# Kernel tuning notes

Measured on AMD Instinct MI355X. Metric: run time of the kernel, lower is better.

## Reference

```python
import jax, jax.numpy as jnp
import numpy as np
import math

N, IN_DIM, Z, H, OUT, K = 16384, 64, 128, 1, 3, 16


def setup_inputs() -> dict:
    key = jax.random.key(0)
    ks = jax.random.split(key, 16)

    def lin(k, din, dout):
        kw, kb = jax.random.split(k)
        W = jax.random.normal(kw, (din, dout), jnp.float32) / math.sqrt(din)
        b = jax.random.normal(kb, (dout,), jnp.float32) * 0.01
        return W, b

    x = jax.random.normal(ks[0], (N, IN_DIM), jnp.float32)
    t = jnp.zeros((1,), jnp.float32)
    # layer dims: (in, heads*out) per TransformerConv
    dims = [(IN_DIM, Z * H), (Z * H, (Z // H) * H), (Z * H, (OUT // H) * H)]
    params = {}
    i = 1
    for li, (din, dout) in enumerate(dims, 1):
        for nm in ("q", "k", "v", "s"):
            W, b = lin(ks[i], din, dout)
            i += 1
            params[f"W{nm}{li}"] = W
            params[f"b{nm}{li}"] = b
    return {"t": t, "x": x, **params}


def knn_edge_index(coo, k):
    # kNN graph on 3-D coords (loop=False): edges neighbor(src) -> center(dst)
    n = coo.shape[0]
    sq = jnp.sum(coo * coo, axis=-1)
    d = sq[:, None] + sq[None, :] - 2.0 * (coo @ coo.T)  # [N, N] sq. distances
    d = d.at[jnp.arange(n), jnp.arange(n)].set(jnp.inf)  # exclude self-loops
    _, idx = jax.lax.top_k(-d, k)  # [N, K] nearest neighbor indices
    src = idx.reshape(-1)
    dst = jnp.repeat(jnp.arange(n), k)
    return src, dst


def tconv(x, src, dst, Wq, bq, Wk, bk, Wv, bv, Ws, bs, heads):
    # PyG TransformerConv (concat=True, root_weight=True, no edge_attr)
    n = x.shape[0]
    dout = Wq.shape[1]
    c = dout // heads
    q = (x @ Wq + bq).reshape(n, heads, c)
    kk = (x @ Wk + bk).reshape(n, heads, c)
    v = (x @ Wv + bv).reshape(n, heads, c)
    alpha = jnp.sum(q[dst] * kk[src], axis=-1) / math.sqrt(c)  # [E, H]
    amax = jax.ops.segment_max(alpha, dst, num_segments=n)
    ex = jnp.exp(alpha - amax[dst])
    denom = jax.ops.segment_sum(ex, dst, num_segments=n)
    w = ex / denom[dst]  # softmax over incoming edges per node
    msg = w[:, :, None] * v[src]  # [E, H, C]
    out = jax.ops.segment_sum(msg, dst, num_segments=n).reshape(n, dout)
    return out + x @ Ws + bs  # root/skip connection


def reference(t, x,
              Wq1, bq1, Wk1, bk1, Wv1, bv1, Ws1, bs1,
              Wq2, bq2, Wk2, bk2, Wv2, bv2, Ws2, bs2,
              Wq3, bq3, Wk3, bk3, Wv3, bv3, Ws3, bs3):
    src, dst = knn_edge_index(x[:, :3], K)  # built under no_grad in original
    h = jnp.tanh(tconv(x, src, dst, Wq1, bq1, Wk1, bk1, Wv1, bv1, Ws1, bs1, H))
    h = jnp.tanh(tconv(h, src, dst, Wq2, bq2, Wk2, bk2, Wv2, bv2, Ws2, bs2, H) + h)
    drift_coo = tconv(h, src, dst, Wq3, bq3, Wk3, bk3, Wv3, bv3, Ws3, bs3, H)
    return drift_coo
```

## Files before the change

kernel.cpp:

```cpp
#include <hip/hip_runtime.h>
#include <math.h>

#define NN 16384
#define CAP 128
#define WM 64
#define KTOP 17
#define NSLAB 128
#define SH 0.0625f
#define SHI 16.0f

typedef unsigned long long u64;

__device__ __forceinline__ int mbcnt64(u64 mask) {
  return __builtin_amdgcn_mbcnt_hi(
      (unsigned)(mask >> 32),
      __builtin_amdgcn_mbcnt_lo((unsigned)mask, 0));
}

__device__ __forceinline__ unsigned fmap(float d) {
  unsigned ub = __float_as_uint(d);
  return ub ^ ((unsigned)((int)ub >> 31) | 0x80000000u);
}

__device__ __forceinline__ float unfmap(unsigned ub) {
  unsigned fb = (ub & 0x80000000u) ? (ub ^ 0x80000000u) : ~ub;
  return __uint_as_float(fb);
}

__device__ __forceinline__ unsigned short f2bf(float f) {
  unsigned u = __float_as_uint(f);
  return (unsigned short)((u + 0x7FFFu + ((u >> 16) & 1u)) >> 16);
}
__device__ __forceinline__ float bf2f(unsigned short h) {
  return __uint_as_float(((unsigned)h) << 16);
}

__device__ __forceinline__ u64 u64min(u64 a, u64 b) { return a < b ? a : b; }
__device__ __forceinline__ u64 u64max(u64 a, u64 b) { return a > b ? a : b; }

__device__ __forceinline__ int slabof(float v) {
  int c = (int)floorf((v + 4.0f) * SHI);
  return c < 0 ? 0 : (c > NSLAB - 1 ? NSLAB - 1 : c);
}

__device__ __forceinline__ void sort64(u64& r0, int lane) {
#pragma unroll
  for (int k = 2; k <= 64; k <<= 1) {
#pragma unroll
    for (int jj = k >> 1; jj >= 1; jj >>= 1) {
      const bool up = (lane & jj) == 0;
      const bool asc = (lane & k) == 0;
      u64 o = __shfl_xor(r0, jj);
      r0 = (up == asc) ? u64min(r0, o) : u64max(r0, o);
    }
  }
}

__device__ __forceinline__ void radix_shrink(u64* buf, int& cnt, float& cq,
                                             int lane) {
  const u64 k0 = (lane < cnt) ? buf[lane] : ~0ull;
  const u64 k1 = (lane + 64 < cnt) ? buf[lane + 64] : ~0ull;
  const unsigned d0 = (unsigned)(k0 >> 32);
  const unsigned d1 = (unsigned)(k1 >> 32);
  unsigned p = 0u;
#pragma unroll
  for (int b = 31; b >= 0; --b) {
    const unsigned c = p | (1u << b);
    const u64 b0 = __ballot(d0 < c);
    const u64 b1 = __ballot(d1 < c);
    const int n = __popcll(b0) + __popcll(b1);
    if (n < KTOP) p = c;
  }
  const bool v0 = d0 <= p;
  const bool v1 = d1 <= p;
  const u64 m0 = __ballot(v0);
  const u64 m1 = __ballot(v1);
  const int base = __popcll(m0);
  if (v0) buf[mbcnt64(m0)] = k0;
  if (v1) buf[base + mbcnt64(m1)] = k1;
  cnt = base + __popcll(m1);
  cq = -unfmap(p);
}

__global__ __launch_bounds__(256) void pack_slabs(const float* __restrict__ x,
                                                  float4* __restrict__ tmp4,
                                                  int* __restrict__ sid,
                                                  unsigned* __restrict__ hist) {
  const int i = blockIdx.x * 256 + threadIdx.x;
  const float a = x[i * 64 + 0];
  const float b = x[i * 64 + 1];
  const float c = x[i * 64 + 2];
  tmp4[i] = make_float4(a, b, c, -0.5f * (a * a + b * b + c * c));
  const int s = slabof(c);
  sid[i] = s;
  atomicAdd(&hist[s], 1u);
}

__global__ __launch_bounds__(128) void prefix_slabs(
    const unsigned* __restrict__ hist, unsigned* __restrict__ slabstart,
    unsigned* __restrict__ slabfill) {
  __shared__ unsigned ls[NSLAB];
  const int t = threadIdx.x;
  const unsigned h = hist[t];
  ls[t] = h;
  __syncthreads();
  for (int off = 1; off < NSLAB; off <<= 1) {
    const unsigned v = (t >= off) ? ls[t - off] : 0u;
    __syncthreads();
    ls[t] += v;
    __syncthreads();
  }
  const unsigned ex = ls[t] - h;
  slabstart[t] = ex;
  slabfill[t] = ex;
  if (t == NSLAB - 1) slabstart[NSLAB] = ls[t];
}

__global__ __launch_bounds__(256) void scatter_slabs(
    const float4* __restrict__ tmp4, const int* __restrict__ sid,
    unsigned* __restrict__ slabfill, float4* __restrict__ sorted4,
    int* __restrict__ sidx) {
  const int i = blockIdx.x * 256 + threadIdx.x;
  const unsigned pos = atomicAdd(&slabfill[sid[i]], 1u);
  sorted4[pos] = tmp4[i];
  sidx[pos] = i;
}

__global__ __launch_bounds__(256) void knn_z(
    const float4* __restrict__ sorted4, const int* __restrict__ sidx,
    const unsigned* __restrict__ slabstart, int* __restrict__ src) {
  __shared__ u64 bufs_[4][CAP];
  const int lane = threadIdx.x & 63;
  const int wid = threadIdx.x >> 6;
  u64* buf = bufs_[wid];
  const int qpos = blockIdx.x * 4 + wid;
  const float4 me = sorted4[qpos];
  const int qorig = sidx[qpos];
  const float qx = me.x, qy = me.y, qz = me.z;
  const float q2 = -2.0f * me.w;
  float cq = -INFINITY;
  int cnt = 0;

  auto scan_run = [&](int s, int e) {
    if (s >= e) return;
    int o = s;
    int j = o + lane;
    float4 p = sorted4[j < e ? j : s];
    while (o < e) {
      const int on = o + 64;
      float4 pn;
      if (on < e) {
        const int jn = on + lane;
        pn = sorted4[jn < e ? jn : s];
      }
      const float L = fmaf(qx, p.x, fmaf(qy, p.y, fmaf(qz, p.z, p.w)));
      const bool pass = (j < e) && (L >= cq);
      const u64 mk = __ballot(pass);
      if (mk) {
        if (pass)
          buf[cnt + mbcnt64(mk)] = ((u64)fmap(-L) << 32) | (unsigned)sidx[j];
        cnt += __popcll(mk);
        if (cnt >= WM) radix_shrink(buf, cnt, cq, lane);
      }
      o = on;
      j = on + lane;
      p = pn;
    }
  };

  const int sq = slabof(qz);
  int su = sq, sd = sq - 1;
  bool up_done = false, dn_done = false;
  while (true) {
    bool can_up = !up_done && su <= NSLAB - 1;
    bool can_dn = !dn_done && sd >= 0;
    float bu = can_up ? fmaxf((-4.0f + su * SH) - qz, 0.0f) : 0.0f;
    float bd = can_dn ? fmaxf(qz - (-4.0f + (sd + 1) * SH), 0.0f) : 0.0f;
    if (cq != -INFINITY) {
      const float d17m =
          fmaxf(fmaf(-2.0f, cq, q2), 0.0f) * 1.00002f + 1e-4f;
      if (can_up && bu * bu > d17m) { can_up = false; up_done = true; }
      if (can_dn && bd * bd > d17m) { can_dn = false; dn_done = true; }
    }
    if (!can_up && !can_dn) {
      if (up_done && dn_done) break;
      if (su > NSLAB - 1 && sd < 0) break;
      if ((up_done || su > NSLAB - 1) && (dn_done || sd < 0)) break;
      break;
    }
    if (can_up && (!can_dn || bu <= bd)) {
      scan_run((int)slabstart[su], (int)slabstart[su + 1]);
      ++su;
    } else {
      scan_run((int)slabstart[sd], (int)slabstart[sd + 1]);
      --sd;
    }
  }

  u64 r0 = (lane < cnt) ? buf[lane] : ~0ull;
  sort64(r0, lane);
  const int idx = (int)(r0 & 0xFFFFFFFFull);
  const u64 selfm = __ballot((lane < KTOP) && (idx == qorig));
  const int sp = selfm ? (__ffsll((long long)selfm) - 1) : 99;
  const int outrank = lane - (lane > sp ? 1 : 0);
  if (lane < KTOP && lane != sp && outrank < 16)
    src[qorig * 16 + outrank] = idx;
}

template <int KD>
__global__ __launch_bounds__(256) void gemm_qkvs(
    const float* __restrict__ X, const float* __restrict__ W0,
    const float* __restrict__ W1, const float* __restrict__ W2,
    const float* __restrict__ W3, const float* __restrict__ B0,
    const float* __restrict__ B1, const float* __restrict__ B2,
    const float* __restrict__ B3, float* __restrict__ qs,
    unsigned short* __restrict__ kvh) {
  __shared__ float As[64][68];
  __shared__ float Bs[64][64];
  const int brow = blockIdx.x * 64;
  const int by = blockIdx.y;
  const int wi = by >> 1;
  const float* W = wi == 0 ? W0 : wi == 1 ? W1 : wi == 2 ? W2 : W3;
  const float* bias = wi == 0 ? B0 : wi == 1 ? B1 : wi == 2 ? B2 : B3;
  const int cbase = (by & 1) * 64;
  const int tx = threadIdx.x & 15;
  const int ty = threadIdx.x >> 4;

  float acc[4][4] = {};
  for (int k0 = 0; k0 < KD; k0 += 64) {
    __syncthreads();
#pragma unroll
    for (int i = 0; i < 4; ++i) {
      const int flat = threadIdx.x * 4 + i * 1024;
      const int r = flat >> 6, kk = flat & 63;
      const float4 v = *(const float4*)&X[(brow + r) * KD + k0 + kk];
      As[kk + 0][r] = v.x;
      As[kk + 1][r] = v.y;
      As[kk + 2][r] = v.z;
      As[kk + 3][r] = v.w;
    }
#pragma unroll
    for (int i = 0; i < 4; ++i) {
      const int flat = threadIdx.x * 4 + i * 1024;
      const int kk = flat >> 6, c = flat & 63;
      *(float4*)&Bs[kk][c] = *(const float4*)&W[(k0 + kk) * 128 + cbase + c];
    }
    __syncthreads();
#pragma unroll 8
    for (int k = 0; k < 64; ++k) {
      const float4 a = *(const float4*)&As[k][ty * 4];
      const float4 b = *(const float4*)&Bs[k][tx * 4];
      const float av[4] = {a.x, a.y, a.z, a.w};
      const float bv[4] = {b.x, b.y, b.z, b.w};
#pragma unroll
      for (int i = 0; i < 4; ++i)
#pragma unroll
        for (int jj = 0; jj < 4; ++jj)
          acc[i][jj] = fmaf(av[i], bv[jj], acc[i][jj]);
    }
  }
  const float4 bi = *(const float4*)&bias[cbase + tx * 4];
  const int col = cbase + tx * 4;
#pragma unroll
  for (int i = 0; i < 4; ++i) {
    const int row = brow + ty * 4 + i;
    float4 o;
    o.x = acc[i][0] + bi.x;
    o.y = acc[i][1] + bi.y;
    o.z = acc[i][2] + bi.z;
    o.w = acc[i][3] + bi.w;
    if (wi == 0) {
      *(float4*)&qs[row * 256 + col] = o;
    } else if (wi == 3) {
      *(float4*)&qs[row * 256 + 128 + col] = o;
    } else {
      ushort4 h;
      h.x = f2bf(o.x);
      h.y = f2bf(o.y);
      h.z = f2bf(o.z);
      h.w = f2bf(o.w);
      *(ushort4*)&kvh[row * 256 + (wi == 1 ? col : 128 + col)] = h;
    }
  }
}

__global__ __launch_bounds__(256) void attn_c128(
    const float* __restrict__ qs, const unsigned short* __restrict__ kvh,
    const int* __restrict__ src, const float* __restrict__ res,
    float* __restrict__ hout, int do_res) {
  const int g = threadIdx.x >> 5;
  const int node = blockIdx.x * 8 + g;
  const int c = threadIdx.x & 31;
  const float4 q4 = ((const float4*)(qs + node * 256))[c];

  int nb[16];
#pragma unroll
  for (int r = 0; r < 16; ++r) nb[r] = src[node * 16 + r];

  float p[16];
#pragma unroll
  for (int r = 0; r < 16; ++r) {
    const ushort4 k4 = ((const ushort4*)(kvh + nb[r] * 256))[c];
    p[r] = q4.x * bf2f(k4.x) + q4.y * bf2f(k4.y) + q4.z * bf2f(k4.z) +
           q4.w * bf2f(k4.w);
  }
#pragma unroll
  for (int o = 16; o; o >>= 1) {
#pragma unroll
    for (int r = 0; r < 16; ++r) p[r] += __shfl_xor(p[r], o);
  }

  float m = p[0];
#pragma unroll
  for (int r = 1; r < 16; ++r) m = fmaxf(m, p[r]);
  float w[16];
  float den = 0.0f;
#pragma unroll
  for (int r = 0; r < 16; ++r) {
    w[r] = __expf((p[r] - m) * 0.088388347648318447f);
    den += w[r];
  }
  const float inv = 1.0f / den;
  float o0 = 0.0f, o1 = 0.0f, o2 = 0.0f, o3 = 0.0f;
#pragma unroll
  for (int r = 0; r < 16; ++r) {
    const ushort4 v4 = ((const ushort4*)(kvh + nb[r] * 256 + 128))[c];
    const float ww = w[r] * inv;
    o0 = fmaf(ww, bf2f(v4.x), o0);
    o1 = fmaf(ww, bf2f(v4.y), o1);
    o2 = fmaf(ww, bf2f(v4.z), o2);
    o3 = fmaf(ww, bf2f(v4.w), o3);
  }
  const float4 s4 = ((const float4*)(qs + node * 256 + 128))[c];
  float r0 = o0 + s4.x, r1 = o1 + s4.y, r2 = o2 + s4.z, r3 = o3 + s4.w;
  if (do_res) {
    const float4 h4 = ((const float4*)(res + node * 128))[c];
    r0 += h4.x;
    r1 += h4.y;
    r2 += h4.z;
    r3 += h4.w;
  }
  ((float4*)(hout + node * 128))[c] =
      make_float4(tanhf(r0), tanhf(r1), tanhf(r2), tanhf(r3));
}

__global__ __launch_bounds__(256) void gemm_qkvs3(
    const float* __restrict__ H, const float* __restrict__ W0,
    const float* __restrict__ W1, const float* __restrict__ W2,
    const float* __restrict__ W3, const float* __restrict__ B0,
    const float* __restrict__ B1, const float* __restrict__ B2,
    const float* __restrict__ B3, float* __restrict__ out) {
  __shared__ float hs[64][132];
  __shared__ float wsh[128 * 12];
  __shared__ float bsh[12];
  const int brow = blockIdx.x * 64;
  if (threadIdx.x < 12) {
    const int mi = threadIdx.x / 3, c = threadIdx.x % 3;
    const float* Bsel = mi == 0 ? B0 : mi == 1 ? B1 : mi == 2 ? B2 : B3;
    bsh[threadIdx.x] = Bsel[c];
  }
  for (int t = threadIdx.x; t < 1536; t += 256) {
    const int k = t / 12, cc = t % 12;
    const int mi = cc / 3, c = cc % 3;
    const float* Wsel = mi == 0 ? W0 : mi == 1 ? W1 : mi == 2 ? W2 : W3;
    wsh[t] = Wsel[k * 3 + c];
  }
#pragma unroll
  for (int i = 0; i < 8; ++i) {
    const int flat = threadIdx.x * 4 + i * 1024;
    const int r = flat >> 7, kk = flat & 127;
    *(float4*)&hs[r][kk] = *(const float4*)&H[(brow + r) * 128 + kk];
  }
  __syncthreads();
  const int r = threadIdx.x >> 2;
  const int part = threadIdx.x & 3;
  float a0 = 0.0f, a1 = 0.0f, a2 = 0.0f;
#pragma unroll 4
  for (int k = 0; k < 128; ++k) {
    const float h = hs[r][k];
    a0 = fmaf(h, wsh[k * 12 + part * 3 + 0], a0);
    a1 = fmaf(h, wsh[k * 12 + part * 3 + 1], a1);
    a2 = fmaf(h, wsh[k * 12 + part * 3 + 2], a2);
  }
  const int row = brow + r;
  out[row * 12 + part * 3 + 0] = a0 + bsh[part * 3 + 0];
  out[row * 12 + part * 3 + 1] = a1 + bsh[part * 3 + 1];
  out[row * 12 + part * 3 + 2] = a2 + bsh[part * 3 + 2];
}

__global__ __launch_bounds__(256) void attn_c3(const float* __restrict__ q3,
                                               const int* __restrict__ src,
                                               float* __restrict__ out) {
  const int gid = blockIdx.x * 256 + threadIdx.x;
  const int node = gid >> 4, r = gid & 15;
  const int j = src[node * 16 + r];
  const float* qn = q3 + node * 12;
  const float* kj = q3 + j * 12 + 3;
  float alpha = (qn[0] * kj[0] + qn[1] * kj[1] + qn[2] * kj[2]) *
                0.57735026918962576f;
  float m = alpha;
#pragma unroll
  for (int o = 8; o; o >>= 1) m = fmaxf(m, __shfl_xor(m, o, 16));
  const float e = __expf(alpha - m);
  float den = e;
#pragma unroll
  for (int o = 8; o; o >>= 1) den += __shfl_xor(den, o, 16);
  const float wgt = e / den;
  const float* vj = q3 + j * 12 + 6;
  float o0 = wgt * vj[0], o1 = wgt * vj[1], o2 = wgt * vj[2];
#pragma unroll
  for (int o = 8; o; o >>= 1) {
    o0 += __shfl_xor(o0, o, 16);
    o1 += __shfl_xor(o1, o, 16);
    o2 += __shfl_xor(o2, o, 16);
  }
  if (r == 0) {
    const float* sn = q3 + node * 12 + 9;
    out[node * 3 + 0] = o0 + sn[0];
    out[node * 3 + 1] = o1 + sn[1];
    out[node * 3 + 2] = o2 + sn[2];
  }
}

extern "C" void kernel_launch(void* const* d_in, const int* in_sizes, int n_in,
                              void* d_out, int out_size, void* d_ws,
                              size_t ws_size, hipStream_t stream) {
  const float* x = (const float*)d_in[1];
  const float* Wq1 = (const float*)d_in[2];
  const float* bq1 = (const float*)d_in[3];
  const float* Wk1 = (const float*)d_in[4];
  const float* bk1 = (const float*)d_in[5];
  const float* Wv1 = (const float*)d_in[6];
  const float* bv1 = (const float*)d_in[7];
  const float* Ws1 = (const float*)d_in[8];
  const float* bs1 = (const float*)d_in[9];
  const float* Wq2 = (const float*)d_in[10];
  const float* bq2 = (const float*)d_in[11];
  const float* Wk2 = (const float*)d_in[12];
  const float* bk2 = (const float*)d_in[13];
  const float* Wv2 = (const float*)d_in[14];
  const float* bv2 = (const float*)d_in[15];
  const float* Ws2 = (const float*)d_in[16];
  const float* bs2 = (const float*)d_in[17];
  const float* Wq3 = (const float*)d_in[18];
  const float* bq3 = (const float*)d_in[19];
  const float* Wk3 = (const float*)d_in[20];
  const float* bk3 = (const float*)d_in[21];
  const float* Wv3 = (const float*)d_in[22];
  const float* bv3 = (const float*)d_in[23];
  const float* Ws3 = (const float*)d_in[24];
  const float* bs3 = (const float*)d_in[25];

  const size_t MB = 1024 * 1024;
  const size_t KB = 1024;
  char* ws = (char*)d_ws;
  float4* tmp4 = (float4*)(ws);
  float4* sorted4 = (float4*)(ws + 256 * KB);
  int* sid = (int*)(ws + 512 * KB);
  int* sidx = (int*)(ws + 576 * KB);
  unsigned* hist = (unsigned*)(ws + 640 * KB);
  unsigned* slabstart = (unsigned*)(ws + 644 * KB);
  unsigned* slabfill = (unsigned*)(ws + 648 * KB);

  float* qs = (float*)(ws);
  unsigned short* kvh = (unsigned short*)(ws + 16 * MB);
  float* h1 = (float*)(ws + 24 * MB);
  float* h2 = (float*)(ws + 32 * MB);
  int* src = (int*)(ws + 40 * MB);
  float* q3 = (float*)(ws + 42 * MB);
  float* out = (float*)d_out;

  hipMemsetAsync(hist, 0, NSLAB * sizeof(unsigned), stream);
  pack_slabs<<<NN / 256, 256, 0, stream>>>(x, tmp4, sid, hist);
  prefix_slabs<<<1, NSLAB, 0, stream>>>(hist, slabstart, slabfill);
  scatter_slabs<<<NN / 256, 256, 0, stream>>>(tmp4, sid, slabfill, sorted4,
                                              sidx);
  knn_z<<<NN / 4, 256, 0, stream>>>(sorted4, sidx, slabstart, src);
  gemm_qkvs<64><<<dim3(NN / 64, 8), 256, 0, stream>>>(
      x, Wq1, Wk1, Wv1, Ws1, bq1, bk1, bv1, bs1, qs, kvh);
  attn_c128<<<NN / 8, 256, 0, stream>>>(qs, kvh, src, nullptr, h1, 0);
  gemm_qkvs<128><<<dim3(NN / 64, 8), 256, 0, stream>>>(
      h1, Wq2, Wk2, Wv2, Ws2, bq2, bk2, bv2, bs2, qs, kvh);
  attn_c128<<<NN / 8, 256, 0, stream>>>(qs, kvh, src, h1, h2, 1);
  gemm_qkvs3<<<NN / 64, 256, 0, stream>>>(h2, Wq3, Wk3, Wv3, Ws3, bq3, bk3,
                                          bv3, bs3, q3);
  attn_c3<<<NN * 16 / 256, 256, 0, stream>>>(q3, src, out);
}
```

Before: 363.2 us.

## Process two adjacent z-sorted queries per wavefront in kNN slab scan

```diff
diff --git a/kernel.cpp b/kernel.cpp
--- a/kernel.cpp
+++ b/kernel.cpp
@@ -129,23 +129,23 @@
 __global__ __launch_bounds__(256) void knn_z(
     const float4* __restrict__ sorted4, const int* __restrict__ sidx,
     const unsigned* __restrict__ slabstart, int* __restrict__ src) {
-  __shared__ u64 bufs_[4][CAP];
+  __shared__ u64 bufs_[4][2][CAP];
   const int lane = threadIdx.x & 63;
   const int wid = threadIdx.x >> 6;
-  u64* buf = bufs_[wid];
-  const int qpos = blockIdx.x * 4 + wid;
-  const float4 me = sorted4[qpos];
-  const int qorig = sidx[qpos];
-  const float qx = me.x, qy = me.y, qz = me.z;
-  const float q2 = -2.0f * me.w;
-  float cq = -INFINITY;
-  int cnt = 0;
-
-  auto scan_run = [&](int s, int e) {
+  u64* buf0 = bufs_[wid][0];
+  u64* buf1 = bufs_[wid][1];
+  const int qpos = blockIdx.x * 8 + wid * 2;
+  const float4 m0 = sorted4[qpos];
+  const float4 m1 = sorted4[qpos + 1];
+  const float qx0 = m0.x, qy0 = m0.y, qz0 = m0.z, q20 = -2.0f * m0.w;
+  const float qx1 = m1.x, qy1 = m1.y, qz1 = m1.z, q21 = -2.0f * m1.w;
+  float cq0 = -INFINITY, cq1 = -INFINITY;
+  int cnt0 = 0, cnt1 = 0;
+
+  auto scan_range = [&](int s, int e) {
     if (s >= e) return;
     int o = s;
-    int j = o + lane;
-    float4 p = sorted4[j < e ? j : s];
+    float4 p = sorted4[(s + lane) < e ? (s + lane) : s];
     while (o < e) {
       const int on = o + 64;
       float4 pn;
@@ -153,58 +153,92 @@
         const int jn = on + lane;
         pn = sorted4[jn < e ? jn : s];
       }
-      const float L = fmaf(qx, p.x, fmaf(qy, p.y, fmaf(qz, p.z, p.w)));
-      const bool pass = (j < e) && (L >= cq);
-      const u64 mk = __ballot(pass);
-      if (mk) {
-        if (pass)
-          buf[cnt + mbcnt64(mk)] = ((u64)fmap(-L) << 32) | (unsigned)sidx[j];
-        cnt += __popcll(mk);
-        if (cnt >= WM) radix_shrink(buf, cnt, cq, lane);
+      const int j = o + lane;
+      const bool in = j < e;
+      const float L0 = fmaf(qx0, p.x, fmaf(qy0, p.y, fmaf(qz0, p.z, p.w)));
+      const float L1 = fmaf(qx1, p.x, fmaf(qy1, p.y, fmaf(qz1, p.z, p.w)));
+      const bool p0 = in && (L0 >= cq0);
+      const bool p1 = in && (L1 >= cq1);
+      const u64 mk0 = __ballot(p0);
+      const u64 mk1 = __ballot(p1);
+      if (mk0 | mk1) {
+        if (mk0) {
+          if (p0)
+            buf0[cnt0 + mbcnt64(mk0)] =
+                ((u64)fmap(-L0) << 32) | (unsigned)sidx[j];
+          cnt0 += __popcll(mk0);
+          if (cnt0 >= WM) radix_shrink(buf0, cnt0, cq0, lane);
+        }
+        if (mk1) {
+          if (p1)
+            buf1[cnt1 + mbcnt64(mk1)] =
+                ((u64)fmap(-L1) << 32) | (unsigned)sidx[j];
+          cnt1 += __popcll(mk1);
+          if (cnt1 >= WM) radix_shrink(buf1, cnt1, cq1, lane);
+        }
       }
       o = on;
-      j = on + lane;
       p = pn;
     }
   };
 
-  const int sq = slabof(qz);
-  int su = sq, sd = sq - 1;
-  bool up_done = false, dn_done = false;
+  int slo = slabof(qz0) - 2;
+  if (slo < 0) slo = 0;
+  int shi = slabof(qz1) + 2;
+  if (shi > NSLAB - 1) shi = NSLAB - 1;
+  scan_range((int)slabstart[slo], (int)slabstart[shi + 1]);
+
+  const float zmin = fminf(qz0, qz1), zmax = fmaxf(qz0, qz1);
   while (true) {
-    bool can_up = !up_done && su <= NSLAB - 1;
-    bool can_dn = !dn_done && sd >= 0;
-    float bu = can_up ? fmaxf((-4.0f + su * SH) - qz, 0.0f) : 0.0f;
-    float bd = can_dn ? fmaxf(qz - (-4.0f + (sd + 1) * SH), 0.0f) : 0.0f;
-    if (cq != -INFINITY) {
-      const float d17m =
-          fmaxf(fmaf(-2.0f, cq, q2), 0.0f) * 1.00002f + 1e-4f;
-      if (can_up && bu * bu > d17m) { can_up = false; up_done = true; }
-      if (can_dn && bd * bd > d17m) { can_dn = false; dn_done = true; }
-    }
-    if (!can_up && !can_dn) {
-      if (up_done && dn_done) break;
-      if (su > NSLAB - 1 && sd < 0) break;
-      if ((up_done || su > NSLAB - 1) && (dn_done || sd < 0)) break;
-      break;
-    }
-    if (can_up && (!can_dn || bu <= bd)) {
-      scan_run((int)slabstart[su], (int)slabstart[su + 1]);
-      ++su;
+    if (cnt0 >= KTOP) radix_shrink(buf0, cnt0, cq0, lane);
+    if (cnt1 >= KTOP) radix_shrink(buf1, cnt1, cq1, lane);
+    int rlo, rhi;
+    if (cnt0 >= KTOP && cnt1 >= KTOP) {
+      const float d0 = fmaxf(fmaf(-2.0f, cq0, q20), 0.0f);
+      const float d1 = fmaxf(fmaf(-2.0f, cq1, q21), 0.0f);
+      const float rneed = sqrtf(fmaxf(d0, d1) * 1.00002f + 1e-4f);
+      rlo = (int)floorf((zmin - rneed + 4.0f) * SHI);
+      rhi = (int)floorf((zmax + rneed + 4.0f) * SHI);
+      if (rlo < 0) rlo = 0;
+      if (rhi > NSLAB - 1) rhi = NSLAB - 1;
+      if (rlo > slo) rlo = slo;
+      if (rhi < shi) rhi = shi;
     } else {
-      scan_run((int)slabstart[sd], (int)slabstart[sd + 1]);
-      --sd;
-    }
-  }
-
-  u64 r0 = (lane < cnt) ? buf[lane] : ~0ull;
-  sort64(r0, lane);
-  const int idx = (int)(r0 & 0xFFFFFFFFull);
-  const u64 selfm = __ballot((lane < KTOP) && (idx == qorig));
-  const int sp = selfm ? (__ffsll((long long)selfm) - 1) : 99;
-  const int outrank = lane - (lane > sp ? 1 : 0);
-  if (lane < KTOP && lane != sp && outrank < 16)
-    src[qorig * 16 + outrank] = idx;
+      rlo = slo - 4;
+      if (rlo < 0) rlo = 0;
+      rhi = shi + 4;
+      if (rhi > NSLAB - 1) rhi = NSLAB - 1;
+    }
+    bool ext = false;
+    if (rlo < slo) {
+      scan_range((int)slabstart[rlo], (int)slabstart[slo]);
+      slo = rlo;
+      ext = true;
+    }
+    if (rhi > shi) {
+      scan_range((int)slabstart[shi + 1], (int)slabstart[rhi + 1]);
+      shi = rhi;
+      ext = true;
+    }
+    if (!ext) break;
+  }
+
+#pragma unroll 1
+  for (int q = 0; q < 2; ++q) {
+    u64* buf = q == 0 ? buf0 : buf1;
+    int cnt = q == 0 ? cnt0 : cnt1;
+    float cqd = q == 0 ? cq0 : cq1;
+    if (cnt > 64) radix_shrink(buf, cnt, cqd, lane);
+    const int qorig = sidx[qpos + q];
+    u64 r0 = (lane < cnt) ? buf[lane] : ~0ull;
+    sort64(r0, lane);
+    const int idx = (int)(r0 & 0xFFFFFFFFull);
+    const u64 selfm = __ballot((lane < KTOP) && (idx == qorig));
+    const int sp = selfm ? (__ffsll((long long)selfm) - 1) : 99;
+    const int outrank = lane - (lane > sp ? 1 : 0);
+    if (lane < KTOP && lane != sp && outrank < 16)
+      src[qorig * 16 + outrank] = idx;
+  }
 }
 
 template <int KD>
@@ -475,7 +509,7 @@
   prefix_slabs<<<1, NSLAB, 0, stream>>>(hist, slabstart, slabfill);
   scatter_slabs<<<NN / 256, 256, 0, stream>>>(tmp4, sid, slabfill, sorted4,
                                               sidx);
-  knn_z<<<NN / 4, 256, 0, stream>>>(sorted4, sidx, slabstart, src);
+  knn_z<<<NN / 8, 256, 0, stream>>>(sorted4, sidx, slabstart, src);
   gemm_qkvs<64><<<dim3(NN / 64, 8), 256, 0, stream>>>(
       x, Wq1, Wk1, Wv1, Ws1, bq1, bk1, bv1, bs1, qs, kvh);
   attn_c128<<<NN / 8, 256, 0, stream>>>(qs, kvh, src, nullptr, h1, 0);
```

New measurement: 358.0 us. No clear change (-1.4%).
